# Kernel tuning notes

Measured on AMD Instinct MI355X. Metric: run time of the kernel, lower is better.

## Reference

```python
import jax, jax.numpy as jnp
import numpy as np

HEADS = 16
DIM_HEAD = 64
QUERY_DIM = 1024
CONTEXT_DIM = 768
INNER = HEADS * DIM_HEAD  # 1024
SCALE = DIM_HEAD ** -0.5


def setup_inputs() -> dict:
    key = jax.random.key(0)
    ks = jax.random.split(key, 7)
    B, Sq, Skv = 4, 2048, 2048
    x = jax.random.normal(ks[0], (B, Sq, QUERY_DIM), dtype=jnp.float32)
    context = jax.random.normal(ks[1], (B, Skv, CONTEXT_DIM), dtype=jnp.float32)
    # Linear weights stored as (in, out) so y = x @ W
    w_q = jax.random.normal(ks[2], (QUERY_DIM, INNER), dtype=jnp.float32) / np.sqrt(QUERY_DIM)
    w_k = jax.random.normal(ks[3], (CONTEXT_DIM, INNER), dtype=jnp.float32) / np.sqrt(CONTEXT_DIM)
    w_v = jax.random.normal(ks[4], (CONTEXT_DIM, INNER), dtype=jnp.float32) / np.sqrt(CONTEXT_DIM)
    w_o = jax.random.normal(ks[5], (INNER, QUERY_DIM), dtype=jnp.float32) / np.sqrt(INNER)
    b_o = jax.random.normal(ks[6], (QUERY_DIM,), dtype=jnp.float32) * 0.02
    return {"x": x, "context": context, "w_q": w_q, "w_k": w_k, "w_v": w_v, "w_o": w_o, "b_o": b_o}


def reference(x, context, w_q, w_k, w_v, w_o, b_o):
    B, Sq, _ = x.shape
    Skv = context.shape[1]
    # projections, split heads: [B, S, H, D] -> [B, H, S, D]
    q = (x @ w_q).reshape(B, Sq, HEADS, DIM_HEAD).transpose(0, 2, 1, 3)
    k = (context @ w_k).reshape(B, Skv, HEADS, DIM_HEAD).transpose(0, 2, 1, 3)
    v = (context @ w_v).reshape(B, Skv, HEADS, DIM_HEAD).transpose(0, 2, 1, 3)
    sim = jnp.einsum('bhid,bhjd->bhij', q, k) * SCALE
    attn = jax.nn.softmax(sim, axis=-1)
    out = jnp.einsum('bhij,bhjd->bhid', attn, v)
    out = out.transpose(0, 2, 1, 3).reshape(B, Sq, INNER)
    return out @ w_o + b_o
```

## Files before the change

kernel.cpp:

```cpp
#include <hip/hip_runtime.h>

typedef __bf16 bf16_t;
typedef __bf16 bf16x8 __attribute__((ext_vector_type(8)));
typedef __bf16 bf16x4 __attribute__((ext_vector_type(4)));
typedef __bf16 bf16x2 __attribute__((ext_vector_type(2)));
typedef float  f32x4  __attribute__((ext_vector_type(4)));
typedef float  f32x16 __attribute__((ext_vector_type(16)));
typedef int    i32x4  __attribute__((ext_vector_type(4)));

#define AS_G(p) ((const __attribute__((address_space(1))) void*)(p))
#define AS_L(p) ((__attribute__((address_space(3))) void*)(p))
#define GLD16(g, l) __builtin_amdgcn_global_load_lds(AS_G(g), AS_L(l), 16, 0, 0)

static __device__ __forceinline__ f32x4 mfma16(bf16x8 a, bf16x8 b, f32x4 c) {
  return __builtin_amdgcn_mfma_f32_16x16x32_bf16(a, b, c, 0, 0, 0);
}
static __device__ __forceinline__ f32x16 mfma32(bf16x8 a, bf16x8 b, f32x16 c) {
  return __builtin_amdgcn_mfma_f32_32x32x16_bf16(a, b, c, 0, 0, 0);
}
static __device__ __forceinline__ int pk2(float a, float b) {
  bf16x2 t; t[0] = (bf16_t)a; t[1] = (bf16_t)b;
  return __builtin_bit_cast(int, t);
}
static __device__ __forceinline__ bf16x8 mk8(int a, int b, int c, int d) {
  i32x4 v{a, b, c, d};
  return __builtin_bit_cast(bf16x8, v);
}
static __device__ __forceinline__ void pl32swap(int& x, int& y) {
  asm volatile("v_permlane32_swap_b32 %0, %1" : "+v"(x), "+v"(y));
}

__global__ __launch_bounds__(256) void cvt_bf16_k(const float* __restrict__ in,
                                                  bf16_t* __restrict__ out, long n) {
  long i = ((long)blockIdx.x * 256 + threadIdx.x) * 4;
  long step = (long)gridDim.x * 256 * 4;
  for (; i < n; i += step) {
    float4 v = *(const float4*)(in + i);
    bf16x4 o;
    o[0] = (bf16_t)v.x; o[1] = (bf16_t)v.y; o[2] = (bf16_t)v.z; o[3] = (bf16_t)v.w;
    *(bf16x4*)(out + i) = o;
  }
}

__global__ __launch_bounds__(256) void tcvt_k(const float* __restrict__ W,
                                              bf16_t* __restrict__ Wt, int K, int N) {
  __shared__ float t[32][33];
  int k0 = blockIdx.y << 5, n0 = blockIdx.x << 5;
  int ti = threadIdx.x >> 3, tj = (threadIdx.x & 7) << 2;
  float4 v = *(const float4*)(W + (size_t)(k0 + ti) * N + n0 + tj);
  t[ti][tj] = v.x; t[ti][tj + 1] = v.y; t[ti][tj + 2] = v.z; t[ti][tj + 3] = v.w;
  __syncthreads();
  bf16x4 o;
  o[0] = (bf16_t)t[tj + 0][ti]; o[1] = (bf16_t)t[tj + 1][ti];
  o[2] = (bf16_t)t[tj + 2][ti]; o[3] = (bf16_t)t[tj + 3][ti];
  *(bf16x4*)(Wt + (size_t)(n0 + ti) * K + k0 + tj) = o;
}

template <int MODE>
__global__ __launch_bounds__(256) void gemm_bt_k(
    const bf16_t* __restrict__ A, const bf16_t* __restrict__ Bt,
    void* __restrict__ Cout, void* __restrict__ Cout2,
    const float* __restrict__ bias, int N, int K, float oscale) {
  __shared__ __align__(16) char lA[8192];
  __shared__ __align__(16) char lB[8192];
  const int tid = threadIdx.x;
  const int lane = tid & 63;
  const int w = tid >> 6;
  const int wr = (w >> 1) << 6;
  const int wc = (w & 1) << 6;
  const long row0 = (long)blockIdx.x << 7;
  const long col0 = (long)blockIdx.y << 7;

  const int r_st = tid >> 2;
  const int cb_st = ((tid & 3) << 4) ^ ((r_st & 3) << 4);
  const char* pa = (const char*)(A + (row0 + r_st) * (long)K) + cb_st;
  const char* pb = (const char*)(Bt + (col0 + r_st) * (long)K) + cb_st;
  const long step64 = (long)K * 128;
  char* la = lA + tid * 16;
  char* lb = lB + tid * 16;

  f32x4 acc[4][4];
#pragma unroll
  for (int m = 0; m < 4; m++)
#pragma unroll
    for (int n = 0; n < 4; n++) acc[m][n] = f32x4{0.f, 0.f, 0.f, 0.f};

  for (int k0 = 0; k0 < K; k0 += 32) {
    __syncthreads();
    GLD16(pa, la); GLD16(pa + step64, la + 4096);
    GLD16(pb, lb); GLD16(pb + step64, lb + 4096);
    __syncthreads();
    pa += 64; pb += 64;
    bf16x8 af[4], bfr[4];
#pragma unroll
    for (int m = 0; m < 4; m++) {
      int row = wr + (m << 4) + (lane & 15);
      int cby = ((lane >> 4) << 4) ^ ((row & 3) << 4);
      af[m] = *(const bf16x8*)(lA + row * 64 + cby);
    }
#pragma unroll
    for (int n = 0; n < 4; n++) {
      int row = wc + (n << 4) + (lane & 15);
      int cby = ((lane >> 4) << 4) ^ ((row & 3) << 4);
      bfr[n] = *(const bf16x8*)(lB + row * 64 + cby);
    }
    __builtin_amdgcn_s_setprio(1);
#pragma unroll
    for (int m = 0; m < 4; m++)
#pragma unroll
      for (int n = 0; n < 4; n++)
        acc[m][n] = mfma16(af[m], bfr[n], acc[m][n]);
    __builtin_amdgcn_s_setprio(0);
  }

  if (MODE == 0) {
    bf16_t* Cb = (bf16_t*)Cout;
#pragma unroll
    for (int n = 0; n < 4; n++) {
      long c = col0 + wc + (n << 4) + (lane & 15);
      long h = c >> 6, d = c & 63;
#pragma unroll
      for (int m = 0; m < 4; m++) {
#pragma unroll
        for (int j = 0; j < 4; j++) {
          long rr = row0 + wr + (m << 4) + ((lane >> 4) << 2) + j;
          long bb = rr >> 11, s = rr & 2047;
          Cb[(((bb << 4) + h) * 2048 + s) * 64 + d] = (bf16_t)(acc[m][n][j] * oscale);
        }
      }
    }
  } else if (MODE == 1) {
    float* Cf = (float*)Cout;
#pragma unroll
    for (int n = 0; n < 4; n++) {
      long c = col0 + wc + (n << 4) + (lane & 15);
      float bv = bias[c];
#pragma unroll
      for (int m = 0; m < 4; m++) {
#pragma unroll
        for (int j = 0; j < 4; j++) {
          long rr = row0 + wr + (m << 4) + ((lane >> 4) << 2) + j;
          Cf[rr * (long)N + c] = acc[m][n][j] + bv;
        }
      }
    }
  } else {
    if (col0 < 1024) {
      bf16_t* Cb = (bf16_t*)Cout;
#pragma unroll
      for (int n = 0; n < 4; n++) {
        long c = col0 + wc + (n << 4) + (lane & 15);
        long h = c >> 6, d = c & 63;
#pragma unroll
        for (int m = 0; m < 4; m++) {
#pragma unroll
          for (int j = 0; j < 4; j++) {
            long rr = row0 + wr + (m << 4) + ((lane >> 4) << 2) + j;
            long bb = rr >> 11, s = rr & 2047;
            Cb[(((bb << 4) + h) * 2048 + s) * 64 + d] = (bf16_t)acc[m][n][j];
          }
        }
      }
    } else {
      bf16_t* Cb = (bf16_t*)Cout2;
#pragma unroll
      for (int n = 0; n < 4; n++) {
        long c = (col0 - 1024) + wc + (n << 4) + (lane & 15);
        long h = c >> 6, d = c & 63;
#pragma unroll
        for (int m = 0; m < 4; m++) {
          long rr = row0 + wr + (m << 4) + ((lane >> 4) << 2);
          long bb = rr >> 11, s = rr & 2047;
          bf16x4 ov;
#pragma unroll
          for (int j = 0; j < 4; j++) ov[j] = (bf16_t)acc[m][n][j];
          *(bf16x4*)(Cb + (((bb << 4) + h) * 64 + d) * 2048 + s) = ov;
        }
      }
    }
  }
}

__global__ __launch_bounds__(256, 3) void attn5_k(
    const bf16_t* __restrict__ Q, const bf16_t* __restrict__ Kh,
    const bf16_t* __restrict__ VT, bf16_t* __restrict__ O) {
  __shared__ __align__(16) char lds_[32768];
  const int tid = threadIdx.x;
  const int lane = tid & 63;
  const int w = tid >> 6;
  const int hi = lane >> 5;
  const int lq = lane & 31;
  const int bh = blockIdx.x;
  const int b = bh >> 4, hh = bh & 15;
  const int q = (blockIdx.y << 7) + (w << 5) + lq;

  const bf16_t* qp = Q + ((size_t)bh * 2048 + q) * 64 + (hi << 3);
  bf16x8 qf[4];
#pragma unroll
  for (int s = 0; s < 4; s++) qf[s] = *(const bf16x8*)(qp + (s << 4));

  const bf16x8 onesf = mk8(0x3F803F80, 0x3F803F80, 0x3F803F80, 0x3F803F80);

  const int r_st = tid >> 3;
  const int csw = ((tid & 7) << 4) ^ ((r_st & 7) << 4);
  const char* pk = (const char*)Kh + (size_t)bh * 262144 + r_st * 128 + csw;
  const char* pv = (const char*)VT + (size_t)bh * 262144 + (size_t)r_st * 4096 + csw;
  const int swz = (lane & 7) << 4;

  f32x16 oa[2], la;
#pragma unroll
  for (int t = 0; t < 2; t++)
#pragma unroll
    for (int r = 0; r < 16; r++) oa[t][r] = 0.f;
#pragma unroll
  for (int r = 0; r < 16; r++) la[r] = 0.f;

  GLD16(pk, lds_ + tid * 16);
  GLD16(pk + 4096, lds_ + 4096 + tid * 16);
  GLD16(pv, lds_ + 8192 + tid * 16);
  GLD16(pv + 131072, lds_ + 12288 + tid * 16);
  __syncthreads();

  for (int it = 0; it < 32; it++) {
    const int buf = it & 1;
    if (it < 31) {
      const char* pkn = pk + (it + 1) * 8192;
      const char* pvn = pv + (it + 1) * 128;
      char* dst = lds_ + ((buf ^ 1) << 14);
      GLD16(pkn, dst + tid * 16);
      GLD16(pkn + 4096, dst + 4096 + tid * 16);
      GLD16(pvn, dst + 8192 + tid * 16);
      GLD16(pvn + 131072, dst + 12288 + tid * 16);
    }
    const char* lk = lds_ + (buf << 14);
    const char* lv = lk + 8192;

    f32x16 sa[2];
#pragma unroll
    for (int h = 0; h < 2; h++) {
#pragma unroll
      for (int r = 0; r < 16; r++) sa[h][r] = 0.f;
      const char* krow = lk + (((h << 5) + lq) << 7);
      __builtin_amdgcn_s_setprio(1);
#pragma unroll
      for (int s = 0; s < 4; s++) {
        bf16x8 kf = *(const bf16x8*)(krow + (((s << 5) + (hi << 4)) ^ swz));
        sa[h] = mfma32(kf, qf[s], sa[h]);
      }
      __builtin_amdgcn_s_setprio(0);
    }

#pragma unroll
    for (int h = 0; h < 2; h++)
#pragma unroll
      for (int r = 0; r < 16; r++)
        sa[h][r] = __builtin_amdgcn_exp2f(sa[h][r]);

    bf16x8 pf[4];
#pragma unroll
    for (int h = 0; h < 2; h++) {
      int x0 = pk2(sa[h][0], sa[h][1]),   y0 = pk2(sa[h][4], sa[h][5]);
      int x1 = pk2(sa[h][2], sa[h][3]),   y1 = pk2(sa[h][6], sa[h][7]);
      pl32swap(x0, y0); pl32swap(x1, y1);
      pf[h * 2 + 0] = mk8(x0, x1, y0, y1);
      int x2 = pk2(sa[h][8], sa[h][9]),   y2 = pk2(sa[h][12], sa[h][13]);
      int x3 = pk2(sa[h][10], sa[h][11]), y3 = pk2(sa[h][14], sa[h][15]);
      pl32swap(x2, y2); pl32swap(x3, y3);
      pf[h * 2 + 1] = mk8(x2, x3, y2, y3);
    }

    __builtin_amdgcn_s_setprio(1);
#pragma unroll
    for (int t = 0; t < 2; t++) {
      const char* vrw = lv + (((t << 5) + lq) << 7);
#pragma unroll
      for (int s = 0; s < 4; s++) {
        bf16x8 vf = *(const bf16x8*)(vrw + (((s << 5) + (hi << 4)) ^ swz));
        oa[t] = mfma32(vf, pf[s], oa[t]);
      }
    }
#pragma unroll
    for (int s = 0; s < 4; s++) la = mfma32(onesf, pf[s], la);
    __builtin_amdgcn_s_setprio(0);
    __syncthreads();
  }

  float invl = 1.f / la[0];
  bf16_t* Ob = O + ((size_t)b * 2048 + q) * 1024 + hh * 64;
#pragma unroll
  for (int t = 0; t < 2; t++)
#pragma unroll
    for (int g = 0; g < 4; g++) {
      bf16x4 ov;
#pragma unroll
      for (int j = 0; j < 4; j++) ov[j] = (bf16_t)(oa[t][(g << 2) + j] * invl);
      *(bf16x4*)(Ob + (t << 5) + (g << 3) + (hi << 2)) = ov;
    }
}

extern "C" void kernel_launch(void* const* d_in, const int* in_sizes, int n_in,
                              void* d_out, int out_size, void* d_ws, size_t ws_size,
                              hipStream_t stream) {
  (void)in_sizes; (void)n_in; (void)out_size; (void)ws_size;
  const float* x   = (const float*)d_in[0];
  const float* ctx = (const float*)d_in[1];
  const float* w_q = (const float*)d_in[2];
  const float* w_k = (const float*)d_in[3];
  const float* w_v = (const float*)d_in[4];
  const float* w_o = (const float*)d_in[5];
  const float* b_o = (const float*)d_in[6];

  char* ws = (char*)d_ws;
  const size_t MB = 1 << 20;
  bf16_t* xb  = (bf16_t*)(ws);
  bf16_t* cb  = (bf16_t*)(ws + 16 * MB);
  bf16_t* wqT = (bf16_t*)(ws + 28 * MB);
  bf16_t* wkT = (bf16_t*)(ws + 30 * MB);
  bf16_t* wvT = (bf16_t*)(ws + 31 * MB + 512 * 1024);
  bf16_t* woT = (bf16_t*)(ws + 33 * MB);
  bf16_t* qws = (bf16_t*)(ws + 35 * MB);
  bf16_t* kws = (bf16_t*)(ws + 51 * MB);
  bf16_t* vtw = (bf16_t*)(ws + 67 * MB);
  bf16_t* ows = xb;

  cvt_bf16_k<<<2048, 256, 0, stream>>>(x, xb, 8388608L);
  cvt_bf16_k<<<2048, 256, 0, stream>>>(ctx, cb, 6291456L);
  tcvt_k<<<dim3(32, 32), 256, 0, stream>>>(w_q, wqT, 1024, 1024);
  tcvt_k<<<dim3(32, 24), 256, 0, stream>>>(w_k, wkT, 768, 1024);
  tcvt_k<<<dim3(32, 24), 256, 0, stream>>>(w_v, wvT, 768, 1024);
  tcvt_k<<<dim3(32, 32), 256, 0, stream>>>(w_o, woT, 1024, 1024);

  const float qs = 0.125f * 1.4426950408889634f;
  gemm_bt_k<0><<<dim3(64, 8), 256, 0, stream>>>(xb, wqT, qws, nullptr, nullptr, 1024, 1024, qs);
  gemm_bt_k<3><<<dim3(64, 16), 256, 0, stream>>>(cb, wkT, kws, vtw, nullptr, 2048, 768, 1.0f);
  attn5_k<<<dim3(64, 16), 256, 0, stream>>>(qws, kws, vtw, ows);
  gemm_bt_k<1><<<dim3(64, 8), 256, 0, stream>>>(ows, woT, d_out, nullptr, b_o, 1024, 1024, 1.0f);
}
```

Before: 204.7 us.

## Merge conversion launches and double GEMM K-tile to 64 with wider swizzle

```diff
diff --git a/kernel.cpp b/kernel.cpp
--- a/kernel.cpp
+++ b/kernel.cpp
@@ -30,22 +30,37 @@
   asm volatile("v_permlane32_swap_b32 %0, %1" : "+v"(x), "+v"(y));
 }
 
-__global__ __launch_bounds__(256) void cvt_bf16_k(const float* __restrict__ in,
-                                                  bf16_t* __restrict__ out, long n) {
+__global__ __launch_bounds__(256) void cvt_all_k(const float* __restrict__ x,
+                                                 bf16_t* __restrict__ xb,
+                                                 const float* __restrict__ ctx,
+                                                 bf16_t* __restrict__ cb,
+                                                 long nx, long ntot) {
   long i = ((long)blockIdx.x * 256 + threadIdx.x) * 4;
   long step = (long)gridDim.x * 256 * 4;
-  for (; i < n; i += step) {
-    float4 v = *(const float4*)(in + i);
+  for (; i < ntot; i += step) {
+    const float* src; bf16_t* dst; long off;
+    if (i < nx) { src = x; dst = xb; off = i; }
+    else        { src = ctx; dst = cb; off = i - nx; }
+    float4 v = *(const float4*)(src + off);
     bf16x4 o;
     o[0] = (bf16_t)v.x; o[1] = (bf16_t)v.y; o[2] = (bf16_t)v.z; o[3] = (bf16_t)v.w;
-    *(bf16x4*)(out + i) = o;
+    *(bf16x4*)(dst + off) = o;
   }
 }
 
-__global__ __launch_bounds__(256) void tcvt_k(const float* __restrict__ W,
-                                              bf16_t* __restrict__ Wt, int K, int N) {
+__global__ __launch_bounds__(256) void tcvt_all_k(
+    const float* __restrict__ w0, const float* __restrict__ w1,
+    const float* __restrict__ w2, const float* __restrict__ w3,
+    bf16_t* __restrict__ t0, bf16_t* __restrict__ t1,
+    bf16_t* __restrict__ t2, bf16_t* __restrict__ t3) {
   __shared__ float t[32][33];
+  const int z = blockIdx.z;
+  const float* W = (z == 0) ? w0 : (z == 1) ? w1 : (z == 2) ? w2 : w3;
+  bf16_t* Wt = (z == 0) ? t0 : (z == 1) ? t1 : (z == 2) ? t2 : t3;
+  const int K = (z == 1 || z == 2) ? 768 : 1024;
+  const int N = 1024;
   int k0 = blockIdx.y << 5, n0 = blockIdx.x << 5;
+  if (k0 >= K) return;
   int ti = threadIdx.x >> 3, tj = (threadIdx.x & 7) << 2;
   float4 v = *(const float4*)(W + (size_t)(k0 + ti) * N + n0 + tj);
   t[ti][tj] = v.x; t[ti][tj + 1] = v.y; t[ti][tj + 2] = v.z; t[ti][tj + 3] = v.w;
@@ -57,12 +72,12 @@
 }
 
 template <int MODE>
-__global__ __launch_bounds__(256) void gemm_bt_k(
+__global__ __launch_bounds__(256, 3) void gemm_bt_k(
     const bf16_t* __restrict__ A, const bf16_t* __restrict__ Bt,
     void* __restrict__ Cout, void* __restrict__ Cout2,
     const float* __restrict__ bias, int N, int K, float oscale) {
-  __shared__ __align__(16) char lA[8192];
-  __shared__ __align__(16) char lB[8192];
+  __shared__ __align__(16) char lA[16384];
+  __shared__ __align__(16) char lB[16384];
   const int tid = threadIdx.x;
   const int lane = tid & 63;
   const int w = tid >> 6;
@@ -71,11 +86,11 @@
   const long row0 = (long)blockIdx.x << 7;
   const long col0 = (long)blockIdx.y << 7;
 
-  const int r_st = tid >> 2;
-  const int cb_st = ((tid & 3) << 4) ^ ((r_st & 3) << 4);
+  const int r_st = tid >> 3;
+  const int cb_st = ((tid & 7) << 4) ^ ((r_st & 7) << 4);
   const char* pa = (const char*)(A + (row0 + r_st) * (long)K) + cb_st;
   const char* pb = (const char*)(Bt + (col0 + r_st) * (long)K) + cb_st;
-  const long step64 = (long)K * 128;
+  const long rowstep = (long)K * 64;
   char* la = lA + tid * 16;
   char* lb = lB + tid * 16;
 
@@ -85,32 +100,38 @@
 #pragma unroll
     for (int n = 0; n < 4; n++) acc[m][n] = f32x4{0.f, 0.f, 0.f, 0.f};
 
-  for (int k0 = 0; k0 < K; k0 += 32) {
+  for (int k0 = 0; k0 < K; k0 += 64) {
     __syncthreads();
-    GLD16(pa, la); GLD16(pa + step64, la + 4096);
-    GLD16(pb, lb); GLD16(pb + step64, lb + 4096);
+#pragma unroll
+    for (int i = 0; i < 4; i++) {
+      GLD16(pa + i * rowstep, la + i * 4096);
+      GLD16(pb + i * rowstep, lb + i * 4096);
+    }
     __syncthreads();
-    pa += 64; pb += 64;
-    bf16x8 af[4], bfr[4];
-#pragma unroll
-    for (int m = 0; m < 4; m++) {
-      int row = wr + (m << 4) + (lane & 15);
-      int cby = ((lane >> 4) << 4) ^ ((row & 3) << 4);
-      af[m] = *(const bf16x8*)(lA + row * 64 + cby);
-    }
-#pragma unroll
-    for (int n = 0; n < 4; n++) {
-      int row = wc + (n << 4) + (lane & 15);
-      int cby = ((lane >> 4) << 4) ^ ((row & 3) << 4);
-      bfr[n] = *(const bf16x8*)(lB + row * 64 + cby);
-    }
-    __builtin_amdgcn_s_setprio(1);
-#pragma unroll
-    for (int m = 0; m < 4; m++)
-#pragma unroll
-      for (int n = 0; n < 4; n++)
-        acc[m][n] = mfma16(af[m], bfr[n], acc[m][n]);
-    __builtin_amdgcn_s_setprio(0);
+    pa += 128; pb += 128;
+#pragma unroll
+    for (int ks = 0; ks < 2; ks++) {
+      bf16x8 af[4], bfr[4];
+#pragma unroll
+      for (int m = 0; m < 4; m++) {
+        int row = wr + (m << 4) + (lane & 15);
+        int cby = ((ks << 6) + ((lane >> 4) << 4)) ^ ((row & 7) << 4);
+        af[m] = *(const bf16x8*)(lA + row * 128 + cby);
+      }
+#pragma unroll
+      for (int n = 0; n < 4; n++) {
+        int row = wc + (n << 4) + (lane & 15);
+        int cby = ((ks << 6) + ((lane >> 4) << 4)) ^ ((row & 7) << 4);
+        bfr[n] = *(const bf16x8*)(lB + row * 128 + cby);
+      }
+      __builtin_amdgcn_s_setprio(1);
+#pragma unroll
+      for (int m = 0; m < 4; m++)
+#pragma unroll
+        for (int n = 0; n < 4; n++)
+          acc[m][n] = mfma16(af[m], bfr[n], acc[m][n]);
+      __builtin_amdgcn_s_setprio(0);
+    }
   }
 
   if (MODE == 0) {
@@ -323,12 +344,8 @@
   bf16_t* vtw = (bf16_t*)(ws + 67 * MB);
   bf16_t* ows = xb;
 
-  cvt_bf16_k<<<2048, 256, 0, stream>>>(x, xb, 8388608L);
-  cvt_bf16_k<<<2048, 256, 0, stream>>>(ctx, cb, 6291456L);
-  tcvt_k<<<dim3(32, 32), 256, 0, stream>>>(w_q, wqT, 1024, 1024);
-  tcvt_k<<<dim3(32, 24), 256, 0, stream>>>(w_k, wkT, 768, 1024);
-  tcvt_k<<<dim3(32, 24), 256, 0, stream>>>(w_v, wvT, 768, 1024);
-  tcvt_k<<<dim3(32, 32), 256, 0, stream>>>(w_o, woT, 1024, 1024);
+  cvt_all_k<<<2048, 256, 0, stream>>>(x, xb, ctx, cb, 8388608L, 14680064L);
+  tcvt_all_k<<<dim3(32, 32, 4), 256, 0, stream>>>(w_q, w_k, w_v, w_o, wqT, wkT, wvT, woT);
 
   const float qs = 0.125f * 1.4426950408889634f;
   gemm_bt_k<0><<<dim3(64, 8), 256, 0, stream>>>(xb, wqT, qws, nullptr, nullptr, 1024, 1024, qs);
```

After: 172.0 us. 1.19x faster.
